# Performance work log

Measured on AMD Instinct MI355X. Metric: run time of the kernel, lower is better.

The kernel has to match this reference:

```python
import jax, jax.numpy as jnp
import numpy as np
import math

H = 512        # hidden_size (channels)
N = 64         # state_size
MAX_LEN = 4096 # kernel length L
BATCH = 8
SEQ = 4096     # seq len of input (== MAX_LEN here)


def _nplr(n):
    # HiPPO-LegS NPLR decomposition (done once at init, numpy float64 for eig stability)
    i = np.arange(n, dtype=np.float64)
    j = np.sqrt(2 * i + 1)
    A = -(np.tril(j[None, :] * j[:, None]) - np.diag(i))
    Bv = j.astype(np.complex128)
    p = j / np.sqrt(2.0)
    w, V = np.linalg.eig(A + p[None, :] * p[:, None])  # normal part; conj-pair eigvals adjacent
    w = w[::2].copy()          # [N/2]
    V = V[:, ::2].copy()       # [N, N/2]
    Bc = V.conj().T @ Bv       # [N/2]
    pc = V.conj().T @ p.astype(np.complex128)
    V_full = np.concatenate([V, V.conj()], axis=-1)      # [N, N]
    VtAV = V_full.conj().T @ A.astype(np.complex128) @ V_full  # [N, N]
    return w, pc, V, Bc, VtAV


def _ri(c):
    # complex -> trailing real/imag pair, float32 (mirrors torch.view_as_real)
    return np.stack([c.real, c.imag], axis=-1).astype(np.float32)


def setup_inputs() -> dict:
    rng = np.random.default_rng(0)
    w, p, V, Bc, Amat = _nplr(N)
    Brep = np.tile(Bc[None, :], (H, 1))                      # [H, N/2]
    C = rng.standard_normal((H, N)).astype(np.complex128)
    C = C @ V.conj()                                         # einsum('hn,nm->hm') -> [H, N/2]
    log_dt = math.log(1e-3) + (math.log(1e-1) - math.log(1e-3)) * rng.random(H)
    dt = np.exp(log_dt)[:, None, None]
    I = np.eye(N, dtype=np.complex128)[None]
    dA = np.linalg.inv(I - dt * Amat / 2) @ (I + dt * Amat / 2)   # [H, N, N]
    dA_power = I - np.linalg.matrix_power(dA, MAX_LEN)
    C2 = np.concatenate([C, C.conj()], axis=-1)              # [H, N]
    C2 = np.einsum('hmn,hm->hn', dA_power.conj(), C2)[:, : N // 2]
    p_rep = np.tile(p[None, None, :], (H, 1, 1))             # [H, 1, N/2]
    Bfull = np.concatenate([Brep[:, None, :], p_rep], axis=1)  # [H, 2, N/2]
    Cfull = np.concatenate([C2[:, None, :], p_rep], axis=1)    # [H, 2, N/2] (q == p)

    key = jax.random.key(0)
    kx, kd = jax.random.split(key)
    return {
        "x": jax.random.normal(kx, (BATCH, SEQ, H), dtype=jnp.float32),
        "log_dt": jnp.asarray(log_dt, dtype=jnp.float32),   # [H]
        "w_ri": jnp.asarray(_ri(w)),                        # [N/2, 2]
        "B_ri": jnp.asarray(_ri(Bfull)),                    # [H, 2, N/2, 2]
        "C_ri": jnp.asarray(_ri(Cfull)),                    # [H, 2, N/2, 2]
        "D": jax.random.normal(kd, (H,), dtype=jnp.float32),
    }


def _s4_kernel(log_dt, w_ri, B_ri, C_ri):
    L = MAX_LEN
    w = w_ri[..., 0] + 1j * w_ri[..., 1]   # [n] with n = N/2
    B = B_ri[..., 0] + 1j * B_ri[..., 1]   # [H, 2, n]
    C = C_ri[..., 0] + 1j * C_ri[..., 1]   # [H, 2, n]
    dt = jnp.exp(log_dt)                   # [H]
    freq = jnp.exp(-2j * jnp.pi / L * jnp.arange(L // 2 + 1))  # [F], F = L/2+1
    z = 2 * (1 - freq) / (1 + freq)        # bilinear-transformed frequencies

    v = C[:, :, None, :].conj() * B[:, None, :, :]   # [H, 2, 2, n]
    wd = w[None, :] * dt[:, None]                    # [H, n]
    # cauchy_mult: r = sum_n v/(z-w) + conj(v)/(z-conj(w)), as batched matmuls over n
    K1 = 1.0 / (z[None, None, :] - wd[:, :, None])          # [H, n, F]
    K2 = 1.0 / (z[None, None, :] - wd.conj()[:, :, None])   # [H, n, F]
    r = jnp.einsum('habn,hnf->habf', v, K1) + jnp.einsum('habn,hnf->habf', v.conj(), K2)
    r = r * dt[:, None, None, None]
    # Woodbury correction for the rank-1 (p, q) augmentation
    k_f = r[:, 0, 0, :] - r[:, 0, 1, :] * r[:, 1, 0, :] / (1 + r[:, 1, 1, :])  # [H, F]
    k_f = k_f * 2 / (1 + freq)
    return jnp.fft.irfft(k_f)   # [H, L]


def reference(x, log_dt, w_ri, B_ri, C_ri, D):
    k = _s4_kernel(log_dt, w_ri, B_ri, C_ri)     # [H, L]
    xt = jnp.transpose(x, (0, 2, 1))             # [B, H, Lx]
    L2 = 2 * MAX_LEN                              # conv pads to 2*kernel_len
    k_f = jnp.fft.rfft(k, n=L2)                  # [H, L2/2+1]
    x_f = jnp.fft.rfft(xt, n=L2)                 # [B, H, L2/2+1]
    y = jnp.fft.irfft(k_f[None] * x_f, n=L2)[..., : xt.shape[-1]]
    y = y + xt * D[None, :, None]                # skip connection
    return jnp.transpose(y, (0, 2, 1))           # [B, Lx, H]
```

## Files before the change

kernel.cpp:

```cpp
#include <hip/hip_runtime.h>
#include <math.h>

#define TPB 256
#define CTPB 512
#define KTPB 512

__device__ __forceinline__ float2 cmul(float2 a, float2 b) {
    return make_float2(a.x * b.x - a.y * b.y, a.x * b.y + a.y * b.x);
}
__device__ __forceinline__ float2 cdivf(float2 a, float2 b) {
    float inv = 1.0f / (b.x * b.x + b.y * b.y);
    return make_float2((a.x * b.x + a.y * b.y) * inv, (a.y * b.x - a.x * b.y) * inv);
}
__device__ __forceinline__ float2 cadd(float2 a, float2 b) { return make_float2(a.x + b.x, a.y + b.y); }
__device__ __forceinline__ float2 csub(float2 a, float2 b) { return make_float2(a.x - b.x, a.y - b.y); }
__device__ __forceinline__ float2 mul_i(float2 a, float d) {
    return make_float2(-d * a.y, d * a.x);
}
__device__ __forceinline__ int brev11(int x) { return (int)(__brev((unsigned)x) >> 21); }
__device__ __forceinline__ int rev8(int x) {
    return ((x & 7) << 9) | (((x >> 3) & 7) << 6) | (((x >> 6) & 7) << 3) | ((x >> 9) & 7);
}
__device__ __forceinline__ int swz(int i) { return i ^ ((i >> 4) & 15) ^ ((i >> 8) & 15); }

__device__ __forceinline__ void dft8(const float2* x, float2* y, float d) {
    const float r = 0.70710678118f;
    float2 s0 = cadd(x[0], x[4]), t0 = csub(x[0], x[4]);
    float2 s1 = cadd(x[1], x[5]), t1 = csub(x[1], x[5]);
    float2 s2 = cadd(x[2], x[6]), t2 = csub(x[2], x[6]);
    float2 s3 = cadd(x[3], x[7]), t3 = csub(x[3], x[7]);
    t1 = cmul(t1, make_float2(r, d * r));
    t2 = mul_i(t2, d);
    t3 = cmul(t3, make_float2(-r, d * r));
    float2 u0 = cadd(s0, s2), v0 = csub(s0, s2);
    float2 u1 = cadd(s1, s3), v1 = mul_i(csub(s1, s3), d);
    y[0] = cadd(u0, u1); y[4] = csub(u0, u1);
    y[2] = cadd(v0, v1); y[6] = csub(v0, v1);
    float2 p0 = cadd(t0, t2), q0 = csub(t0, t2);
    float2 p1 = cadd(t1, t3), q1 = mul_i(csub(t1, t3), d);
    y[1] = cadd(p0, p1); y[5] = csub(p0, p1);
    y[3] = cadd(q0, q1); y[7] = csub(q0, q1);
}

__device__ __forceinline__ void dft8z(float2 x0, float2 x1, float2 x2, float2 x3,
                                      float2* y, float d) {
    const float r = 0.70710678118f;
    float2 u0 = cadd(x0, x2), v0 = csub(x0, x2);
    float2 u1 = cadd(x1, x3), v1 = mul_i(csub(x1, x3), d);
    float2 t1 = cmul(x1, make_float2(r, d * r));
    float2 t2 = mul_i(x2, d);
    float2 t3 = cmul(x3, make_float2(-r, d * r));
    float2 p0 = cadd(x0, t2), q0 = csub(x0, t2);
    float2 p1 = cadd(t1, t3), q1 = mul_i(csub(t1, t3), d);
    y[0] = cadd(u0, u1); y[4] = csub(u0, u1);
    y[2] = cadd(v0, v1); y[6] = csub(v0, v1);
    y[1] = cadd(p0, p1); y[5] = csub(p0, p1);
    y[3] = cadd(q0, q1); y[7] = csub(q0, q1);
}

__device__ __forceinline__ void dft8_lo(const float2* x, float2* y, float d) {
    const float r = 0.70710678118f;
    float2 s0 = cadd(x[0], x[4]), t0 = csub(x[0], x[4]);
    float2 s1 = cadd(x[1], x[5]), t1 = csub(x[1], x[5]);
    float2 s2 = cadd(x[2], x[6]), t2 = csub(x[2], x[6]);
    float2 s3 = cadd(x[3], x[7]), t3 = csub(x[3], x[7]);
    t1 = cmul(t1, make_float2(r, d * r));
    t2 = mul_i(t2, d);
    t3 = cmul(t3, make_float2(-r, d * r));
    float2 u0 = cadd(s0, s2), v0 = csub(s0, s2);
    float2 u1 = cadd(s1, s3), v1 = mul_i(csub(s1, s3), d);
    y[0] = cadd(u0, u1);
    y[2] = cadd(v0, v1);
    float2 p0 = cadd(t0, t2), q0 = csub(t0, t2);
    float2 p1 = cadd(t1, t3), q1 = mul_i(csub(t1, t3), d);
    y[1] = cadd(p0, p1);
    y[3] = cadd(q0, q1);
}

template <int HB, int DIR>
__device__ __forceinline__ void dif_stage(float2* s, int tid) {
    __syncthreads();
    const int h = 1 << HB;
    int j = tid & (h - 1);
    int base = ((tid >> HB) << (HB + 3)) + j;
    int s0 = swz(base);
    float2 x[8];
#pragma unroll
    for (int k = 0; k < 8; ++k) x[k] = s[s0 ^ swz(k << HB)];
    float2 y[8];
    dft8(x, y, (float)DIR);
    if constexpr (HB != 0) {
        float ang = (float)DIR * 6.283185307179586f / (float)(h << 3) * (float)j;
        float c, sn;
        __sincosf(ang, &sn, &c);
        float2 w = make_float2(c, sn), wm = w;
        s[s0] = y[0];
#pragma unroll
        for (int m = 1; m < 8; ++m) {
            s[s0 ^ swz(m << HB)] = cmul(wm, y[m]);
            wm = cmul(wm, w);
        }
    } else {
#pragma unroll
        for (int m = 0; m < 8; ++m) s[s0 ^ swz(m << HB)] = y[m];
    }
}

template <int HB, int DIR>
__device__ __forceinline__ void dit_stage(float2* s, int tid) {
    __syncthreads();
    const int h = 1 << HB;
    int j = tid & (h - 1);
    int base = ((tid >> HB) << (HB + 3)) + j;
    int s0 = swz(base);
    float2 x[8];
    if constexpr (HB != 0) {
        float ang = (float)DIR * 6.283185307179586f / (float)(h << 3) * (float)j;
        float c, sn;
        __sincosf(ang, &sn, &c);
        float2 w = make_float2(c, sn);
        x[0] = s[s0];
        float2 wm = w;
#pragma unroll
        for (int k = 1; k < 8; ++k) {
            x[k] = cmul(wm, s[s0 ^ swz(k << HB)]);
            wm = cmul(wm, w);
        }
    } else {
#pragma unroll
        for (int k = 0; k < 8; ++k) x[k] = s[s0 ^ swz(k << HB)];
    }
    float2 y[8];
    dft8(x, y, (float)DIR);
#pragma unroll
    for (int m = 0; m < 8; ++m) s[s0 ^ swz(m << HB)] = y[m];
}

template <int LOGN, int NT>
__device__ void fft8_dif(float2* s, int tid, float dir) {
    const int N = 1 << LOGN;
#pragma unroll
    for (int hb = LOGN - 3; hb >= 0; hb -= 3) {
        const int h = 1 << hb;
        const float astep = dir * 6.283185307179586f / (float)(h << 3);
        __syncthreads();
#pragma unroll
        for (int it = 0; it < (N >> 3) / NT; ++it) {
            const int b = tid + it * NT;
            int j = b & (h - 1);
            int base = ((b >> hb) << (hb + 3)) + j;
            int s0 = swz(base);
            float2 x[8];
#pragma unroll
            for (int k = 0; k < 8; ++k) x[k] = s[s0 ^ swz(k << hb)];
            float2 y[8];
            dft8(x, y, dir);
            if (hb != 0) {
                float ang = astep * (float)j;
                float c, sn;
                __sincosf(ang, &sn, &c);
                float2 w = make_float2(c, sn), wm = w;
                s[s0] = y[0];
#pragma unroll
                for (int m = 1; m < 8; ++m) {
                    s[s0 ^ swz(m << hb)] = cmul(wm, y[m]);
                    wm = cmul(wm, w);
                }
            } else {
#pragma unroll
                for (int m = 0; m < 8; ++m) s[s0 ^ swz(m << hb)] = y[m];
            }
        }
    }
    __syncthreads();
}

template <int LOGN, int NT>
__device__ void fft_dif2(float2* s, int tid, float dir) {
    const int N = 1 << LOGN;
    for (int st = LOGN - 1; st >= 0; --st) {
        __syncthreads();
        int half = 1 << st;
        for (int b = tid; b < (N >> 1); b += NT) {
            int j  = b & (half - 1);
            int i0 = ((b >> st) << (st + 1)) + j;
            int i1 = i0 + half;
            float2 u = s[i0], v = s[i1];
            float2 d = make_float2(u.x - v.x, u.y - v.y);
            s[i0] = make_float2(u.x + v.x, u.y + v.y);
            if (half > 1) {
                float ang = dir * 3.14159265358979f * (float)j / (float)half;
                float c, sn;
                __sincosf(ang, &sn, &c);
                s[i1] = cmul(make_float2(c, sn), d);
            } else {
                s[i1] = d;
            }
        }
    }
    __syncthreads();
}

__global__ __launch_bounds__(KTPB) void prep_kernel(
    const float* __restrict__ log_dt, const float* __restrict__ w_ri,
    const float* __restrict__ Bri, const float* __restrict__ Cri,
    const float* __restrict__ x, float2* __restrict__ Kt, float* __restrict__ xt) {
    __shared__ float2 s[4096];
    __shared__ float2 kf_last;
    __shared__ float2 wds[32];
    __shared__ float aab[4][32], rab[4][32];
    __shared__ float qn[32], pn[32];
    const int tid = threadIdx.x;

    if (blockIdx.x >= 512) {
        float* tile = (float*)s;
        const int tl_id = blockIdx.x - 512;
        const int b  = tl_id >> 9;
        const int rem = tl_id & 511;
        const int t0 = (rem >> 3) << 6;
        const int h0 = (rem & 7) << 6;
        const float4* xv = (const float4*)(x + ((size_t)b * 4096 + t0) * 512 + h0);
#pragma unroll
        for (int i = 0; i < 2; ++i) {
            int idx = tid + KTPB * i;
            int tl = idx >> 4, hq = idx & 15;
            float4 v = xv[(size_t)tl * 128 + hq];
            tile[tl * 65 + hq * 4 + 0] = v.x; tile[tl * 65 + hq * 4 + 1] = v.y;
            tile[tl * 65 + hq * 4 + 2] = v.z; tile[tl * 65 + hq * 4 + 3] = v.w;
        }
        __syncthreads();
        float* xo = xt + ((size_t)(b * 512 + h0)) * 4096 + t0;
#pragma unroll
        for (int i = 0; i < 2; ++i) {
            int idx = tid + KTPB * i;
            int hl = idx >> 4, tq = idx & 15;
            float4 v = make_float4(tile[(tq * 4 + 0) * 65 + hl], tile[(tq * 4 + 1) * 65 + hl],
                                   tile[(tq * 4 + 2) * 65 + hl], tile[(tq * 4 + 3) * 65 + hl]);
            ((float4*)(xo + (size_t)hl * 4096))[tq] = v;
        }
        return;
    }

    const int hh = blockIdx.x;
    float2* kfs = s + 2048;
    const float dt = expf(log_dt[hh]);
    if (tid < 32) {
        float wr = w_ri[2 * tid] * dt, wi = w_ri[2 * tid + 1] * dt;
        wds[tid] = make_float2(wr, wi);
        qn[tid]  = wr * wr + wi * wi;
        pn[tid]  = -2.0f * wr;
    }
    __syncthreads();
    if (tid < 128) {
        int a = tid >> 6, b = (tid >> 5) & 1, n = tid & 31;
        const float* Cp = Cri + (((hh * 2 + a) * 32) + n) * 2;
        const float* Bp = Bri + (((hh * 2 + b) * 32) + n) * 2;
        float Cr = Cp[0], Ci = Cp[1], Br = Bp[0], Bi = Bp[1];
        float2 v = make_float2(Cr * Br + Ci * Bi, Cr * Bi - Ci * Br);
        float2 wd = wds[n];
        aab[a * 2 + b][n] = -2.0f * (v.x * wd.x + v.y * wd.y);
        rab[a * 2 + b][n] = 2.0f * v.x;
    }
    __syncthreads();
    for (int f = tid; f < 2049; f += KTPB) {
        float th = (6.283185307179586f / 4096.0f) * (float)f;
        float cf = cosf(th), sf = sinf(th);
        float2 den = make_float2(1.0f + cf, -sf);
        float zt  = 2.0f * tanf(0.5f * th);
        float zt2 = zt * zt;
        float2 r00 = make_float2(0.f, 0.f), r01 = r00, r10 = r00, r11 = r00;
        for (int n = 0; n < 32; ++n) {
            float c   = qn[n] - zt2;
            float d   = pn[n] * zt;
            float inv = 1.0f / (c * c + d * d);
            float cc = c * inv, dd = d * inv;
            float a0 = aab[0][n], b0 = rab[0][n] * zt;
            r00.x += a0 * cc + b0 * dd; r00.y += b0 * cc - a0 * dd;
            float a1 = aab[1][n], b1 = rab[1][n] * zt;
            r01.x += a1 * cc + b1 * dd; r01.y += b1 * cc - a1 * dd;
            float a2 = aab[2][n], b2 = rab[2][n] * zt;
            r10.x += a2 * cc + b2 * dd; r10.y += b2 * cc - a2 * dd;
            float a3 = aab[3][n], b3 = rab[3][n] * zt;
            r11.x += a3 * cc + b3 * dd; r11.y += b3 * cc - a3 * dd;
        }
        r00.x *= dt; r00.y *= dt; r01.x *= dt; r01.y *= dt;
        r10.x *= dt; r10.y *= dt; r11.x *= dt; r11.y *= dt;
        float2 q  = cdivf(cmul(r01, r10), make_float2(1.0f + r11.x, r11.y));
        float2 k0 = make_float2(r00.x - q.x, r00.y - q.y);
        float2 kv = cmul(k0, cdivf(make_float2(2.0f, 0.0f), den));
        if (f < 2048) kfs[f] = kv; else kf_last = kv;
    }
    __syncthreads();

    for (int m = tid; m < 2048; m += KTPB) {
        float2 Xm = kfs[m];
        float2 Xc = (m == 0) ? kf_last : kfs[2048 - m];
        if (m == 0) { Xm.y = 0.0f; Xc.y = 0.0f; }
        float2 A  = make_float2(Xm.x + Xc.x, Xm.y - Xc.y);
        float2 Bv = make_float2(Xm.x - Xc.x, Xm.y + Xc.y);
        float ang = (3.14159265358979f / 2048.0f) * (float)m;
        float c, sn;
        __sincosf(ang, &sn, &c);
        float2 O = cmul(make_float2(c, sn), Bv);
        s[m] = make_float2(0.5f * (A.x - O.y), 0.5f * (A.y + O.x));
    }
    fft_dif2<11, KTPB>(s, tid, +1.0f);
    float2 reg[4];
    const float sc = 1.0f / 2048.0f;
#pragma unroll
    for (int i = 0; i < 4; ++i) {
        int t = tid + KTPB * i;
        float2 v = s[brev11(t)];
        reg[i] = make_float2(v.x * sc, v.y * sc);
    }
    __syncthreads();
#pragma unroll
    for (int i = 0; i < 4; ++i) {
        int t = tid + KTPB * i;
        s[swz(t)]        = reg[i];
        s[swz(t + 2048)] = make_float2(0.f, 0.f);
    }
    fft8_dif<12, KTPB>(s, tid, -1.0f);
    float2* K = Kt + (size_t)hh * 4097;
    for (int p = tid; p < 4096; p += KTPB) {
        int j  = rev8(p);
        int jc = (4096 - j) & 4095;
        int pc = rev8(jc);
        float2 Yj = s[swz(p)], Yc = s[swz(pc)];
        float2 A  = make_float2(Yj.x + Yc.x, Yj.y - Yc.y);
        float2 Bv = make_float2(Yj.x - Yc.x, Yj.y + Yc.y);
        float ang = -(3.14159265358979f / 4096.0f) * (float)j;
        float c, sn;
        __sincosf(ang, &sn, &c);
        float2 t2 = cmul(make_float2(c, sn), make_float2(Bv.y, -Bv.x));
        K[p] = make_float2(0.5f * (A.x + t2.x), 0.5f * (A.y + t2.y));
        if (p == 0) K[4096] = make_float2(Yj.x - Yj.y, 0.0f);
    }
}

__global__ __launch_bounds__(CTPB) void conv_kernel(const float* xt,
                                                    const float2* __restrict__ Kt,
                                                    const float* __restrict__ Dv,
                                                    float* yt) {
    __shared__ float2 s[4096];
    const int row = blockIdx.x, tid = threadIdx.x;
    const int hch = row & 511;
    const int stid = swz(tid);
    const float2* xr = (const float2*)(xt + (size_t)row * 4096);

    {
        float2 x0 = xr[tid], x1 = xr[tid + 512], x2 = xr[tid + 1024], x3 = xr[tid + 1536];
        float2 y[8];
        dft8z(x0, x1, x2, x3, y, -1.0f);
        float ang = -(6.283185307179586f / 4096.0f) * (float)tid;
        float c, sn;
        __sincosf(ang, &sn, &c);
        float2 w = make_float2(c, sn), wm = w;
        s[stid] = y[0];
#pragma unroll
        for (int m = 1; m < 8; ++m) {
            s[stid ^ swz(m << 9)] = cmul(wm, y[m]);
            wm = cmul(wm, w);
        }
    }
    dif_stage<6, -1>(s, tid);
    dif_stage<3, -1>(s, tid);
    dif_stage<0, -1>(s, tid);
    __syncthreads();
    const float2* K = Kt + (size_t)hch * 4097;
#pragma unroll
    for (int i = 0; i < 8; ++i) {
        int p  = tid + CTPB * i;
        int sp = stid ^ swz(CTPB * i);
        if (p == 0) {
            float2 Y0 = s[sp];
            float X0 = Y0.x + Y0.y;
            float Xn = Y0.x - Y0.y;
            float Z0 = X0 * K[0].x;
            float Zn = Xn * K[4096].x;
            s[sp] = make_float2(0.5f * (Z0 + Zn), 0.5f * (Z0 - Zn));
            continue;
        }
        int j  = rev8(p);
        int jc = 4096 - j;
        int pc = rev8(jc & 4095);
        if (pc < p) continue;
        float2 Yj = s[sp], Yc = s[swz(pc)];
        float2 A  = make_float2(Yj.x + Yc.x, Yj.y - Yc.y);
        float2 Bv = make_float2(Yj.x - Yc.x, Yj.y + Yc.y);
        float ang = -(3.14159265358979f / 4096.0f) * (float)j;
        float c, sn;
        __sincosf(ang, &sn, &c);
        float2 W = make_float2(c, sn);
        float2 t2 = cmul(W, make_float2(Bv.y, -Bv.x));
        float2 Xj = make_float2(0.5f * (A.x + t2.x), 0.5f * (A.y + t2.y));
        float2 t2c = cmul(make_float2(-W.x, W.y), make_float2(Bv.y, Bv.x));
        float2 Xc2 = make_float2(0.5f * (A.x + t2c.x), 0.5f * (-A.y + t2c.y));
        float2 Zj = cmul(Xj, K[p]);
        float2 Zc = cmul(Xc2, K[pc]);
        float2 A2 = make_float2(Zj.x + Zc.x, Zj.y - Zc.y);
        float2 B2 = make_float2(Zj.x - Zc.x, Zj.y + Zc.y);
        float2 O2 = cmul(make_float2(W.x, -W.y), B2);
        s[sp] = make_float2(0.5f * (A2.x - O2.y), 0.5f * (A2.y + O2.x));
        if (pc != p) {
            float2 O2c = cmul(make_float2(-W.x, -W.y), make_float2(-B2.x, B2.y));
            s[swz(pc)] = make_float2(0.5f * (A2.x - O2c.y), 0.5f * (-A2.y + O2c.x));
        }
    }
    dit_stage<0, 1>(s, tid);
    dit_stage<3, 1>(s, tid);
    dit_stage<6, 1>(s, tid);
    __syncthreads();
    {
        float ang = (6.283185307179586f / 4096.0f) * (float)tid;
        float c, sn;
        __sincosf(ang, &sn, &c);
        float2 w = make_float2(c, sn);
        float2 x[8];
        x[0] = s[stid];
        float2 wm = w;
#pragma unroll
        for (int k = 1; k < 8; ++k) {
            x[k] = cmul(wm, s[stid ^ swz(k << 9)]);
            wm = cmul(wm, w);
        }
        float2 y[4];
        dft8_lo(x, y, 1.0f);
        const float D = Dv[hch];
        float2* yo = (float2*)(yt + (size_t)row * 4096);
        const float sc = 1.0f / 4096.0f;
#pragma unroll
        for (int m = 0; m < 4; ++m) {
            int t2 = tid + (m << 9);
            float2 xin = xr[t2];
            yo[t2] = make_float2(y[m].x * sc + D * xin.x, y[m].y * sc + D * xin.y);
        }
    }
}

__global__ __launch_bounds__(TPB) void transpose_out(const float* __restrict__ yt,
                                                     float* __restrict__ out) {
    __shared__ float tile[64][65];
    const int b = blockIdx.z, t0 = blockIdx.y * 64, h0 = blockIdx.x * 64;
    const int tid = threadIdx.x;
    const float* yp = yt + ((size_t)(b * 512 + h0)) * 4096 + t0;
#pragma unroll
    for (int i = 0; i < 4; ++i) {
        int idx = tid + TPB * i;
        int hl = idx >> 4, tq = idx & 15;
        float4 v = ((const float4*)(yp + (size_t)hl * 4096))[tq];
        tile[tq * 4 + 0][hl] = v.x; tile[tq * 4 + 1][hl] = v.y;
        tile[tq * 4 + 2][hl] = v.z; tile[tq * 4 + 3][hl] = v.w;
    }
    __syncthreads();
    float4* ov = (float4*)(out + ((size_t)b * 4096 + t0) * 512 + h0);
#pragma unroll
    for (int i = 0; i < 4; ++i) {
        int idx = tid + TPB * i;
        int tl = idx >> 4, hq = idx & 15;
        float4 v = make_float4(tile[tl][4 * hq + 0], tile[tl][4 * hq + 1],
                               tile[tl][4 * hq + 2], tile[tl][4 * hq + 3]);
        ov[(size_t)tl * 128 + hq] = v;
    }
}

extern "C" void kernel_launch(void* const* d_in, const int* in_sizes, int n_in,
                              void* d_out, int out_size, void* d_ws, size_t ws_size,
                              hipStream_t stream) {
    (void)in_sizes; (void)n_in; (void)out_size; (void)ws_size;
    const float* x      = (const float*)d_in[0];
    const float* log_dt = (const float*)d_in[1];
    const float* w_ri   = (const float*)d_in[2];
    const float* Bri    = (const float*)d_in[3];
    const float* Cri    = (const float*)d_in[4];
    const float* Dv     = (const float*)d_in[5];
    float* out = (float*)d_out;

    char* ws = (char*)d_ws;
    float*  xt = (float*)(ws);
    float2* Kt = (float2*)(ws + 67108864);

    prep_kernel<<<512 + 4096, KTPB, 0, stream>>>(log_dt, w_ri, Bri, Cri, x, Kt, xt);
    conv_kernel<<<4096, CTPB, 0, stream>>>(xt, Kt, Dv, xt);
    transpose_out<<<dim3(8, 64, 8), TPB, 0, stream>>>(xt, out);
}
```

Baseline: 260.7 us.

## Pack two batch rows into one complex 8192-point FFT for convolution

The convolution used a real-FFT trick that packed even/odd samples of one row into a 4096-point complex FFT, which needed a split/merge post-processing pass with twiddles and conjugate pairs. It now packs two batch rows (real and imaginary parts) into a single 8192-point complex FFT. The kernel spectrum is precomputed as a full 8192-point Hermitian-extended array with the scaling folded in, so the frequency-domain step becomes a plain pointwise multiply. Blocks grow to 1024 threads with 64 KB of shared memory and half as many blocks. This trades the split/merge arithmetic for a larger FFT per block, which may lower occupancy, and doubles the kernel-spectrum storage.

Measured after the change: 293.9 us. 12.7% more time.

```diff
diff --git a/kernel.cpp b/kernel.cpp
--- a/kernel.cpp
+++ b/kernel.cpp
@@ -2,7 +2,7 @@
 #include <math.h>
 
 #define TPB 256
-#define CTPB 512
+#define CTPB 1024
 #define KTPB 512
 
 __device__ __forceinline__ float2 cmul(float2 a, float2 b) {
@@ -22,6 +22,9 @@
     return ((x & 7) << 9) | (((x >> 3) & 7) << 6) | (((x >> 6) & 7) << 3) | ((x >> 9) & 7);
 }
 __device__ __forceinline__ int swz(int i) { return i ^ ((i >> 4) & 15) ^ ((i >> 8) & 15); }
+__device__ __forceinline__ int swz13(int i) {
+    return i ^ ((i >> 4) & 15) ^ ((i >> 8) & 15) ^ ((i >> 12) & 1);
+}
 
 __device__ __forceinline__ void dft8(const float2* x, float2* y, float d) {
     const float r = 0.70710678118f;
@@ -78,62 +81,52 @@
 }
 
 template <int HB, int DIR>
-__device__ __forceinline__ void dif_stage(float2* s, int tid) {
+__device__ __forceinline__ void dif13(float2* s, int tid) {
     __syncthreads();
     const int h = 1 << HB;
     int j = tid & (h - 1);
     int base = ((tid >> HB) << (HB + 3)) + j;
-    int s0 = swz(base);
+    int s0 = swz13(base);
     float2 x[8];
 #pragma unroll
-    for (int k = 0; k < 8; ++k) x[k] = s[s0 ^ swz(k << HB)];
+    for (int k = 0; k < 8; ++k) x[k] = s[s0 ^ swz13(k << HB)];
     float2 y[8];
     dft8(x, y, (float)DIR);
-    if constexpr (HB != 0) {
-        float ang = (float)DIR * 6.283185307179586f / (float)(h << 3) * (float)j;
-        float c, sn;
-        __sincosf(ang, &sn, &c);
-        float2 w = make_float2(c, sn), wm = w;
-        s[s0] = y[0];
-#pragma unroll
-        for (int m = 1; m < 8; ++m) {
-            s[s0 ^ swz(m << HB)] = cmul(wm, y[m]);
-            wm = cmul(wm, w);
-        }
-    } else {
-#pragma unroll
-        for (int m = 0; m < 8; ++m) s[s0 ^ swz(m << HB)] = y[m];
+    float ang = (float)DIR * 6.283185307179586f / (float)(h << 3) * (float)j;
+    float c, sn;
+    __sincosf(ang, &sn, &c);
+    float2 w = make_float2(c, sn), wm = w;
+    s[s0] = y[0];
+#pragma unroll
+    for (int m = 1; m < 8; ++m) {
+        s[s0 ^ swz13(m << HB)] = cmul(wm, y[m]);
+        wm = cmul(wm, w);
     }
 }
 
 template <int HB, int DIR>
-__device__ __forceinline__ void dit_stage(float2* s, int tid) {
+__device__ __forceinline__ void dit13(float2* s, int tid) {
     __syncthreads();
     const int h = 1 << HB;
     int j = tid & (h - 1);
     int base = ((tid >> HB) << (HB + 3)) + j;
-    int s0 = swz(base);
+    int s0 = swz13(base);
+    float ang = (float)DIR * 6.283185307179586f / (float)(h << 3) * (float)j;
+    float c, sn;
+    __sincosf(ang, &sn, &c);
+    float2 w = make_float2(c, sn);
     float2 x[8];
-    if constexpr (HB != 0) {
-        float ang = (float)DIR * 6.283185307179586f / (float)(h << 3) * (float)j;
-        float c, sn;
-        __sincosf(ang, &sn, &c);
-        float2 w = make_float2(c, sn);
-        x[0] = s[s0];
-        float2 wm = w;
-#pragma unroll
-        for (int k = 1; k < 8; ++k) {
-            x[k] = cmul(wm, s[s0 ^ swz(k << HB)]);
-            wm = cmul(wm, w);
-        }
-    } else {
-#pragma unroll
-        for (int k = 0; k < 8; ++k) x[k] = s[s0 ^ swz(k << HB)];
+    x[0] = s[s0];
+    float2 wm = w;
+#pragma unroll
+    for (int k = 1; k < 8; ++k) {
+        x[k] = cmul(wm, s[s0 ^ swz13(k << HB)]);
+        wm = cmul(wm, w);
     }
     float2 y[8];
     dft8(x, y, (float)DIR);
 #pragma unroll
-    for (int m = 0; m < 8; ++m) s[s0 ^ swz(m << HB)] = y[m];
+    for (int m = 0; m < 8; ++m) s[s0 ^ swz13(m << HB)] = y[m];
 }
 
 template <int LOGN, int NT>
@@ -321,20 +314,32 @@
         s[swz(t + 2048)] = make_float2(0.f, 0.f);
     }
     fft8_dif<12, KTPB>(s, tid, -1.0f);
-    float2* K = Kt + (size_t)hh * 4097;
-    for (int p = tid; p < 4096; p += KTPB) {
-        int j  = rev8(p);
-        int jc = (4096 - j) & 4095;
-        int pc = rev8(jc);
-        float2 Yj = s[swz(p)], Yc = s[swz(pc)];
-        float2 A  = make_float2(Yj.x + Yc.x, Yj.y - Yc.y);
-        float2 Bv = make_float2(Yj.x - Yc.x, Yj.y + Yc.y);
-        float ang = -(3.14159265358979f / 4096.0f) * (float)j;
-        float c, sn;
-        __sincosf(ang, &sn, &c);
-        float2 t2 = cmul(make_float2(c, sn), make_float2(Bv.y, -Bv.x));
-        K[p] = make_float2(0.5f * (A.x + t2.x), 0.5f * (A.y + t2.y));
-        if (p == 0) K[4096] = make_float2(Yj.x - Yj.y, 0.0f);
+    float2* K2 = Kt + ((size_t)hh << 13);
+    const float isc = 1.0f / 8192.0f;
+    const float2 Y0 = s[swz(0)];
+    const float nyq = Y0.x - Y0.y;
+    for (int q = tid; q < 8192; q += KTPB) {
+        int j13 = ((q >> 10) & 7) | (((q >> 7) & 7) << 3) | (((q >> 4) & 7) << 6)
+                | (((q >> 1) & 7) << 9) | ((q & 1) << 12);
+        int cj = j13 > 4096;
+        int j  = cj ? 8192 - j13 : j13;
+        float2 X;
+        if (j == 4096) {
+            X = make_float2(nyq, 0.0f);
+        } else {
+            int p  = rev8(j);
+            int pc = rev8((4096 - j) & 4095);
+            float2 Yj = s[swz(p)], Yc = s[swz(pc)];
+            float2 A  = make_float2(Yj.x + Yc.x, Yj.y - Yc.y);
+            float2 Bv = make_float2(Yj.x - Yc.x, Yj.y + Yc.y);
+            float ang = -(3.14159265358979f / 4096.0f) * (float)j;
+            float c, sn;
+            __sincosf(ang, &sn, &c);
+            float2 t2 = cmul(make_float2(c, sn), make_float2(Bv.y, -Bv.x));
+            X = make_float2(0.5f * (A.x + t2.x), 0.5f * (A.y + t2.y));
+        }
+        if (cj) X.y = -X.y;
+        K2[q] = make_float2(X.x * isc, X.y * isc);
     }
 }
 
@@ -342,77 +347,69 @@
                                                     const float2* __restrict__ Kt,
                                                     const float* __restrict__ Dv,
                                                     float* yt) {
-    __shared__ float2 s[4096];
-    const int row = blockIdx.x, tid = threadIdx.x;
-    const int hch = row & 511;
-    const int stid = swz(tid);
-    const float2* xr = (const float2*)(xt + (size_t)row * 4096);
+    __shared__ float2 s[8192];
+    const int bp  = blockIdx.x >> 9;
+    const int hch = blockIdx.x & 511;
+    const int tid = threadIdx.x;
+    const int stid = swz13(tid);
+    float* r1 = (float*)(xt + ((size_t)(bp * 1024 + hch)) * 4096);
+    float* r2 = r1 + (size_t)512 * 4096;
 
     {
-        float2 x0 = xr[tid], x1 = xr[tid + 512], x2 = xr[tid + 1024], x3 = xr[tid + 1536];
+        float2 z[4];
+#pragma unroll
+        for (int k = 0; k < 4; ++k) {
+            int t = tid + (k << 10);
+            z[k] = make_float2(r1[t], r2[t]);
+        }
         float2 y[8];
-        dft8z(x0, x1, x2, x3, y, -1.0f);
-        float ang = -(6.283185307179586f / 4096.0f) * (float)tid;
+        dft8z(z[0], z[1], z[2], z[3], y, -1.0f);
+        float ang = -(6.283185307179586f / 8192.0f) * (float)tid;
         float c, sn;
         __sincosf(ang, &sn, &c);
         float2 w = make_float2(c, sn), wm = w;
         s[stid] = y[0];
 #pragma unroll
         for (int m = 1; m < 8; ++m) {
-            s[stid ^ swz(m << 9)] = cmul(wm, y[m]);
+            s[stid ^ swz13(m << 10)] = cmul(wm, y[m]);
             wm = cmul(wm, w);
         }
     }
-    dif_stage<6, -1>(s, tid);
-    dif_stage<3, -1>(s, tid);
-    dif_stage<0, -1>(s, tid);
-    __syncthreads();
-    const float2* K = Kt + (size_t)hch * 4097;
+    dif13<7, -1>(s, tid);
+    dif13<4, -1>(s, tid);
+    dif13<1, -1>(s, tid);
+    __syncthreads();
+#pragma unroll
+    for (int it = 0; it < 4; ++it) {
+        int b  = tid + (it << 10);
+        int i0 = swz13(b << 1), i1 = swz13((b << 1) | 1);
+        float2 u = s[i0], v = s[i1];
+        s[i0] = cadd(u, v);
+        s[i1] = csub(u, v);
+    }
+    __syncthreads();
+    const float2* K = Kt + ((size_t)hch << 13);
 #pragma unroll
     for (int i = 0; i < 8; ++i) {
-        int p  = tid + CTPB * i;
-        int sp = stid ^ swz(CTPB * i);
-        if (p == 0) {
-            float2 Y0 = s[sp];
-            float X0 = Y0.x + Y0.y;
-            float Xn = Y0.x - Y0.y;
-            float Z0 = X0 * K[0].x;
-            float Zn = Xn * K[4096].x;
-            s[sp] = make_float2(0.5f * (Z0 + Zn), 0.5f * (Z0 - Zn));
-            continue;
-        }
-        int j  = rev8(p);
-        int jc = 4096 - j;
-        int pc = rev8(jc & 4095);
-        if (pc < p) continue;
-        float2 Yj = s[sp], Yc = s[swz(pc)];
-        float2 A  = make_float2(Yj.x + Yc.x, Yj.y - Yc.y);
-        float2 Bv = make_float2(Yj.x - Yc.x, Yj.y + Yc.y);
-        float ang = -(3.14159265358979f / 4096.0f) * (float)j;
-        float c, sn;
-        __sincosf(ang, &sn, &c);
-        float2 W = make_float2(c, sn);
-        float2 t2 = cmul(W, make_float2(Bv.y, -Bv.x));
-        float2 Xj = make_float2(0.5f * (A.x + t2.x), 0.5f * (A.y + t2.y));
-        float2 t2c = cmul(make_float2(-W.x, W.y), make_float2(Bv.y, Bv.x));
-        float2 Xc2 = make_float2(0.5f * (A.x + t2c.x), 0.5f * (-A.y + t2c.y));
-        float2 Zj = cmul(Xj, K[p]);
-        float2 Zc = cmul(Xc2, K[pc]);
-        float2 A2 = make_float2(Zj.x + Zc.x, Zj.y - Zc.y);
-        float2 B2 = make_float2(Zj.x - Zc.x, Zj.y + Zc.y);
-        float2 O2 = cmul(make_float2(W.x, -W.y), B2);
-        s[sp] = make_float2(0.5f * (A2.x - O2.y), 0.5f * (A2.y + O2.x));
-        if (pc != p) {
-            float2 O2c = cmul(make_float2(-W.x, -W.y), make_float2(-B2.x, B2.y));
-            s[swz(pc)] = make_float2(0.5f * (A2.x - O2c.y), 0.5f * (-A2.y + O2c.x));
-        }
-    }
-    dit_stage<0, 1>(s, tid);
-    dit_stage<3, 1>(s, tid);
-    dit_stage<6, 1>(s, tid);
+        int p  = tid + (i << 10);
+        int sp = stid ^ swz13(i << 10);
+        s[sp] = cmul(s[sp], K[p]);
+    }
+    __syncthreads();
+#pragma unroll
+    for (int it = 0; it < 4; ++it) {
+        int b  = tid + (it << 10);
+        int i0 = swz13(b << 1), i1 = swz13((b << 1) | 1);
+        float2 u = s[i0], v = s[i1];
+        s[i0] = cadd(u, v);
+        s[i1] = csub(u, v);
+    }
+    dit13<1, 1>(s, tid);
+    dit13<4, 1>(s, tid);
+    dit13<7, 1>(s, tid);
     __syncthreads();
     {
-        float ang = (6.283185307179586f / 4096.0f) * (float)tid;
+        float ang = (6.283185307179586f / 8192.0f) * (float)tid;
         float c, sn;
         __sincosf(ang, &sn, &c);
         float2 w = make_float2(c, sn);
@@ -421,19 +418,18 @@
         float2 wm = w;
 #pragma unroll
         for (int k = 1; k < 8; ++k) {
-            x[k] = cmul(wm, s[stid ^ swz(k << 9)]);
+            x[k] = cmul(wm, s[stid ^ swz13(k << 10)]);
             wm = cmul(wm, w);
         }
         float2 y[4];
         dft8_lo(x, y, 1.0f);
         const float D = Dv[hch];
-        float2* yo = (float2*)(yt + (size_t)row * 4096);
-        const float sc = 1.0f / 4096.0f;
 #pragma unroll
         for (int m = 0; m < 4; ++m) {
-            int t2 = tid + (m << 9);
-            float2 xin = xr[t2];
-            yo[t2] = make_float2(y[m].x * sc + D * xin.x, y[m].y * sc + D * xin.y);
+            int t = tid + (m << 10);
+            float x1 = r1[t], x2 = r2[t];
+            r1[t] = y[m].x + D * x1;
+            r2[t] = y[m].y + D * x2;
         }
     }
 }
@@ -481,6 +477,6 @@
     float2* Kt = (float2*)(ws + 67108864);
 
     prep_kernel<<<512 + 4096, KTPB, 0, stream>>>(log_dt, w_ri, Bri, Cri, x, Kt, xt);
-    conv_kernel<<<4096, CTPB, 0, stream>>>(xt, Kt, Dv, xt);
+    conv_kernel<<<2048, CTPB, 0, stream>>>(xt, Kt, Dv, xt);
     transpose_out<<<dim3(8, 64, 8), TPB, 0, stream>>>(xt, out);
 }
```
